# Kernel optimization log

Hardware: AMD Instinct MI355X
Metric: run time of the kernel (lower is better)

Reference implementation:

```python
import jax, jax.numpy as jnp
import numpy as np

N_NODES = 50000
N_EDGES = 800000
D = 96

def setup_inputs() -> dict:
    key = jax.random.key(0)
    ks = jax.random.split(key, 8)
    g = 0.1  # glorot-ish scale
    return {
        "x": jax.random.normal(ks[0], (N_NODES, D), jnp.float32),
        "edge_index": jax.random.randint(ks[1], (2, N_EDGES), 0, N_NODES, jnp.int64),
        "W1_root": jax.random.normal(ks[2], (D, D), jnp.float32) * g,
        "W1_nbr": jax.random.normal(ks[3], (D, D), jnp.float32) * g,
        "b1": jnp.zeros((D,), jnp.float32),
        "W2_root": jax.random.normal(ks[4], (D, D), jnp.float32) * g,
        "W2_nbr": jax.random.normal(ks[5], (D, D), jnp.float32) * g,
        "b2": jnp.zeros((D,), jnp.float32),
        "lin_w": jax.random.normal(ks[6], (D, 2 * D), jnp.float32) * g,
        "lin_b": jnp.zeros((D,), jnp.float32),
    }

def _conv(h, src, dst, W_root, W_nbr, b, neighbor_norm):
    # gather messages from source nodes, scatter-add into destination nodes
    agg = jax.ops.segment_sum(h[src], dst, num_segments=N_NODES)  # [N, D]
    if neighbor_norm:
        deg = jax.ops.segment_sum(jnp.ones_like(dst, dtype=h.dtype), dst,
                                  num_segments=N_NODES)
        agg = agg / jnp.maximum(deg, 1.0)[:, None]
    return h @ W_root + agg @ W_nbr + b

def reference(x, edge_index, W1_root, W1_nbr, b1, W2_root, W2_nbr, b2, lin_w, lin_b):
    src, dst = edge_index[0], edge_index[1]
    h1 = _conv(x, src, dst, W1_root, W1_nbr, b1, neighbor_norm=False)  # conv1, norm='None'
    h2 = _conv(h1, src, dst, W2_root, W2_nbr, b2, neighbor_norm=True)  # conv, neighbornorm
    # dropout is identity in eval mode; out=False so no global pooling
    cat = jnp.concatenate([h1, h2], axis=-1)  # [N, 2D]
    return jax.nn.relu(cat @ lin_w.T + lin_b)
```

## Files before the change

kernel.cpp:

```cpp
#include <hip/hip_runtime.h>

#define DN 96
#define NCHUNK 256

typedef __attribute__((ext_vector_type(8))) short bf16x8;
typedef __attribute__((ext_vector_type(4))) float f32x4;

__device__ __forceinline__ int edge_at(const void* ei, long long idx, int use64) {
    if (use64) return (int)((const long long*)ei)[idx];
    return ((const int*)ei)[idx];
}

__device__ __forceinline__ unsigned short f2bf(float f) {
    unsigned int u = __float_as_uint(f);
    return (unsigned short)((u + 0x7fffu + ((u >> 16) & 1u)) >> 16);
}

__global__ __launch_bounds__(256) void preprocess(
        const float* __restrict__ x, unsigned int* __restrict__ xb,
        const void* __restrict__ ei, unsigned int* __restrict__ eidx,
        int* __restrict__ hist,
        const float* __restrict__ W1r, const float* __restrict__ W1n,
        const float* __restrict__ W2r, const float* __restrict__ W2n,
        const float* __restrict__ lw, unsigned short* __restrict__ WT,
        long long E, long long CE, int nbuck, int NP) {
    __shared__ int lh[800];
    __shared__ int flag;
    int c = blockIdx.x, tid = threadIdx.x;

    if (tid == 0) flag = 1;
    for (int b = tid; b < nbuck; b += 256) lh[b] = 0;
    __syncthreads();
    if (((const unsigned int*)ei)[2 * tid + 1] != 0u) atomicAnd(&flag, 0);
    __syncthreads();
    int use64 = flag;

    long long beg = (long long)c * CE;
    long long end = beg + CE; if (end > E) end = E;
    for (long long e = beg + tid; e < end; e += 256) {
        int s = edge_at(ei, e, use64);
        int d = edge_at(ei, E + e, use64);
        eidx[e] = (unsigned int)s | ((unsigned int)d << 16);
        atomicAdd(&lh[d >> 6], 1);
    }
    __syncthreads();
    for (int b = tid; b < nbuck; b += 256)
        hist[(size_t)c * nbuck + b] = lh[b];

    int gstride = gridDim.x * 256;
    for (int i = c * 256 + tid; i < NP; i += gstride) {
        float2 v = *(const float2*)(x + 2 * (size_t)i);
        xb[i] = (unsigned int)f2bf(v.x) | ((unsigned int)f2bf(v.y) << 16);
    }

    for (int j = c * 256 + tid; j < 3 * DN * 192; j += gstride) {
        int w = j / (DN * 192);
        int r = j % (DN * 192);
        int jj = r / 192, k = r % 192;
        float v;
        if (w == 0)      v = (k < DN) ? W1r[(size_t)k * DN + jj] : W1n[(size_t)(k - DN) * DN + jj];
        else if (w == 1) v = (k < DN) ? W2r[(size_t)k * DN + jj] : W2n[(size_t)(k - DN) * DN + jj];
        else             v = lw[r];
        WT[j] = f2bf(v);
    }
}

__global__ void bucket_scan(const int* __restrict__ hist, int* __restrict__ pos_rel,
                            int* __restrict__ btot, int nbuck) {
    __shared__ int wsum[4];
    int b = blockIdx.x, tid = threadIdx.x;
    int lane = tid & 63, wid = tid >> 6;
    int v = hist[(size_t)tid * nbuck + b];
    int sv = v;
#pragma unroll
    for (int off = 1; off < 64; off <<= 1) {
        int t = __shfl_up(sv, off, 64);
        if (lane >= off) sv += t;
    }
    if (lane == 63) wsum[wid] = sv;
    __syncthreads();
    int woff = 0;
    for (int w = 0; w < wid; ++w) woff += wsum[w];
    pos_rel[(size_t)tid * nbuck + b] = woff + sv - v;
    if (tid == 255) btot[b] = woff + sv;
}

__global__ void scan_excl(int* data, int n) {
    __shared__ int swsum[16];
    int tid = threadIdx.x;
    int lane = tid & 63, wid = tid >> 6;
    int carry = 0;
    for (int base = 0; base < n; base += 1024) {
        int i = base + tid;
        int v = (i < n) ? data[i] : 0;
        int sv = v;
#pragma unroll
        for (int off = 1; off < 64; off <<= 1) {
            int t = __shfl_up(sv, off, 64);
            if (lane >= off) sv += t;
        }
        __syncthreads();
        if (lane == 63) swsum[wid] = sv;
        __syncthreads();
        if (tid < 16) {
            int wv = swsum[tid];
#pragma unroll
            for (int off = 1; off < 16; off <<= 1) {
                int t = __shfl_up(wv, off, 16);
                if (tid >= off) wv += t;
            }
            swsum[tid] = wv;
        }
        __syncthreads();
        int woff = (wid > 0) ? swsum[wid - 1] : 0;
        int excl = carry + woff + sv - v;
        if (i < n) data[i] = excl;
        carry += swsum[15];
        __syncthreads();
    }
    if (tid == 0) data[n] = carry;
}

__global__ void scatter_grouped(const unsigned int* __restrict__ eidx, long long E,
                                const int* __restrict__ pos_rel,
                                const int* __restrict__ bstart,
                                unsigned int* __restrict__ packed,
                                int nbuck, long long CE) {
    __shared__ int cur[800];
    int c = blockIdx.x, tid = threadIdx.x;
    for (int b = tid; b < nbuck; b += 256)
        cur[b] = pos_rel[(size_t)c * nbuck + b] + bstart[b];
    __syncthreads();
    long long beg = (long long)c * CE;
    long long end = beg + CE; if (end > E) end = E;
    for (long long e = beg + tid; e < end; e += 256) {
        unsigned int u = eidx[e];
        int src = (int)(u & 0xFFFFu);
        int dst = (int)(u >> 16);
        int b = dst >> 6;
        int p = atomicAdd(&cur[b], 1);
        packed[p] = (unsigned int)src | ((unsigned int)(dst & 63) << 16);
    }
}

__global__ void bucket_sort(const unsigned int* __restrict__ packed,
                            const int* __restrict__ bstart,
                            unsigned short* __restrict__ csr_src,
                            int* __restrict__ rowptr, int n, int nbuck) {
    __shared__ int bin[64];
    __shared__ int cur[64];
    int b = blockIdx.x, tid = threadIdx.x;
    int beg = bstart[b], end = bstart[b + 1];
    if (tid < 64) bin[tid] = 0;
    __syncthreads();
    for (int i = beg + tid; i < end; i += 256)
        atomicAdd(&bin[packed[i] >> 16], 1);
    __syncthreads();
    if (tid < 64) {
        int v = bin[tid];
        int sv = v;
#pragma unroll
        for (int off = 1; off < 64; off <<= 1) {
            int t = __shfl_up(sv, off, 64);
            if (tid >= off) sv += t;
        }
        int excl = sv - v;
        cur[tid] = beg + excl;
        int node = b * 64 + tid;
        if (node < n) rowptr[node] = beg + excl;
    }
    __syncthreads();
    for (int i = beg + tid; i < end; i += 256) {
        unsigned int p = packed[i];
        int q = atomicAdd(&cur[p >> 16], 1);
        csr_src[q] = (unsigned short)(p & 0xFFFFu);
    }
    if (b == nbuck - 1 && tid == 0) rowptr[n] = end;
}

__device__ __forceinline__ void acc_row(float* acc, uint4 v) {
    unsigned int u;
    u = v.x; acc[0] += __uint_as_float(u << 16); acc[1] += __uint_as_float(u & 0xffff0000u);
    u = v.y; acc[2] += __uint_as_float(u << 16); acc[3] += __uint_as_float(u & 0xffff0000u);
    u = v.z; acc[4] += __uint_as_float(u << 16); acc[5] += __uint_as_float(u & 0xffff0000u);
    u = v.w; acc[6] += __uint_as_float(u << 16); acc[7] += __uint_as_float(u & 0xffff0000u);
}

__global__ void aggregate(const unsigned int* __restrict__ in, unsigned int* __restrict__ out,
                          const int* __restrict__ rowptr,
                          const unsigned short* __restrict__ srcs,
                          int n, int normalize) {
    int t = blockIdx.x * blockDim.x + threadIdx.x;
    if (t >= n * 12) return;
    int node = t / 12, c = t % 12;
    int beg = rowptr[node], end = rowptr[node + 1];
    float acc[8];
#pragma unroll
    for (int j = 0; j < 8; ++j) acc[j] = 0.f;
    int i = beg;
    for (; i + 4 <= end; i += 4) {
        int s0 = srcs[i], s1 = srcs[i + 1], s2 = srcs[i + 2], s3 = srcs[i + 3];
        uint4 v0 = *(const uint4*)(in + (size_t)s0 * 48 + c * 4);
        uint4 v1 = *(const uint4*)(in + (size_t)s1 * 48 + c * 4);
        uint4 v2 = *(const uint4*)(in + (size_t)s2 * 48 + c * 4);
        uint4 v3 = *(const uint4*)(in + (size_t)s3 * 48 + c * 4);
        acc_row(acc, v0); acc_row(acc, v1); acc_row(acc, v2); acc_row(acc, v3);
    }
    for (; i < end; ++i) {
        uint4 v = *(const uint4*)(in + (size_t)srcs[i] * 48 + c * 4);
        acc_row(acc, v);
    }
    if (normalize) {
        float inv = 1.0f / fmaxf((float)(end - beg), 1.0f);
#pragma unroll
        for (int j = 0; j < 8; ++j) acc[j] *= inv;
    }
    uint4 r;
    r.x = (unsigned int)f2bf(acc[0]) | ((unsigned int)f2bf(acc[1]) << 16);
    r.y = (unsigned int)f2bf(acc[2]) | ((unsigned int)f2bf(acc[3]) << 16);
    r.z = (unsigned int)f2bf(acc[4]) | ((unsigned int)f2bf(acc[5]) << 16);
    r.w = (unsigned int)f2bf(acc[6]) | ((unsigned int)f2bf(acc[7]) << 16);
    *(uint4*)(out + (size_t)node * 48 + c * 4) = r;
}

__global__ __launch_bounds__(256) void gemm_mfma(
        const unsigned short* __restrict__ Abf, const unsigned short* __restrict__ Bbf,
        const unsigned short* __restrict__ WT, const float* __restrict__ bias,
        float* __restrict__ outf, unsigned short* __restrict__ outb,
        int n, int dorelu) {
    __shared__ unsigned int WTl[DN * 100];
    int tid = threadIdx.x;
    const unsigned int* WTg = (const unsigned int*)WT;
    for (int i = tid; i < DN * 96; i += 256) {
        int j = i / 96, m = i - j * 96;
        WTl[j * 100 + m] = WTg[i];
    }
    __syncthreads();

    int wid = tid >> 6, lane = tid & 63;
    int lg = lane >> 4, lr = lane & 15;
    int rowbase = blockIdx.x * 128 + wid * 32;

    f32x4 acc[2][6];
#pragma unroll
    for (int rt = 0; rt < 2; ++rt)
#pragma unroll
        for (int ct = 0; ct < 6; ++ct) acc[rt][ct] = (f32x4){0.f, 0.f, 0.f, 0.f};

    const unsigned short* WTs = (const unsigned short*)WTl;
#pragma unroll
    for (int kt = 0; kt < 6; ++kt) {
        const unsigned short* src = (kt < 3) ? Abf : Bbf;
        int kk = (kt < 3 ? kt : kt - 3) * 32 + lg * 8;
        bf16x8 afrag[2];
#pragma unroll
        for (int rt = 0; rt < 2; ++rt) {
            int row = rowbase + rt * 16 + lr;
            if (row >= n) row = n - 1;
            afrag[rt] = *(const bf16x8*)(src + (size_t)row * DN + kk);
        }
        int koff = kt * 32 + lg * 8;
#pragma unroll
        for (int ct = 0; ct < 6; ++ct) {
            bf16x8 bfrag = *(const bf16x8*)(WTs + (ct * 16 + lr) * 200 + koff);
            acc[0][ct] = __builtin_amdgcn_mfma_f32_16x16x32_bf16(afrag[0], bfrag, acc[0][ct], 0, 0, 0);
            acc[1][ct] = __builtin_amdgcn_mfma_f32_16x16x32_bf16(afrag[1], bfrag, acc[1][ct], 0, 0, 0);
        }
    }

#pragma unroll
    for (int ct = 0; ct < 6; ++ct) {
        int col = ct * 16 + lr;
        float bv = bias[col];
#pragma unroll
        for (int rt = 0; rt < 2; ++rt)
#pragma unroll
            for (int r = 0; r < 4; ++r) {
                int row = rowbase + rt * 16 + lg * 4 + r;
                if (row < n) {
                    float v = acc[rt][ct][r] + bv;
                    if (dorelu) v = fmaxf(v, 0.f);
                    if (outf) outf[(size_t)row * DN + col] = v;
                    if (outb) outb[(size_t)row * DN + col] = f2bf(v);
                }
            }
    }
}

__global__ __launch_bounds__(256) void gemm_fused(
        const unsigned short* __restrict__ h1, const unsigned short* __restrict__ agg,
        const unsigned short* __restrict__ WT2, const float* __restrict__ b2,
        const unsigned short* __restrict__ WT3, const float* __restrict__ lb,
        float* __restrict__ out, int n) {
    __shared__ unsigned int WTl[DN * 100];
    __shared__ unsigned short h2t[4][32][98];
    int tid = threadIdx.x, wid = tid >> 6, lane = tid & 63;
    int lg = lane >> 4, lr = lane & 15;
    int rowbase = blockIdx.x * 128 + wid * 32;

    const unsigned int* WTg2 = (const unsigned int*)WT2;
    for (int i = tid; i < DN * 96; i += 256) {
        int j = i / 96, m = i - j * 96;
        WTl[j * 100 + m] = WTg2[i];
    }
    __syncthreads();

    f32x4 acc[2][6];
#pragma unroll
    for (int rt = 0; rt < 2; ++rt)
#pragma unroll
        for (int ct = 0; ct < 6; ++ct) acc[rt][ct] = (f32x4){0.f, 0.f, 0.f, 0.f};

    const unsigned short* WTs = (const unsigned short*)WTl;
    bf16x8 afragA[2][3];
#pragma unroll
    for (int kt = 0; kt < 6; ++kt) {
        bf16x8 afrag[2];
#pragma unroll
        for (int rt = 0; rt < 2; ++rt) {
            int row = rowbase + rt * 16 + lr;
            if (row >= n) row = n - 1;
            if (kt < 3) {
                afrag[rt] = *(const bf16x8*)(h1 + (size_t)row * DN + kt * 32 + lg * 8);
                afragA[rt][kt] = afrag[rt];
            } else {
                afrag[rt] = *(const bf16x8*)(agg + (size_t)row * DN + (kt - 3) * 32 + lg * 8);
            }
        }
        int koff = kt * 32 + lg * 8;
#pragma unroll
        for (int ct = 0; ct < 6; ++ct) {
            bf16x8 bfrag = *(const bf16x8*)(WTs + (ct * 16 + lr) * 200 + koff);
            acc[0][ct] = __builtin_amdgcn_mfma_f32_16x16x32_bf16(afrag[0], bfrag, acc[0][ct], 0, 0, 0);
            acc[1][ct] = __builtin_amdgcn_mfma_f32_16x16x32_bf16(afrag[1], bfrag, acc[1][ct], 0, 0, 0);
        }
    }

#pragma unroll
    for (int ct = 0; ct < 6; ++ct) {
        float bv = b2[ct * 16 + lr];
#pragma unroll
        for (int rt = 0; rt < 2; ++rt)
#pragma unroll
            for (int r = 0; r < 4; ++r)
                h2t[wid][rt * 16 + lg * 4 + r][ct * 16 + lr] = f2bf(acc[rt][ct][r] + bv);
    }
    __syncthreads();

    const unsigned int* WTg3 = (const unsigned int*)WT3;
    for (int i = tid; i < DN * 96; i += 256) {
        int j = i / 96, m = i - j * 96;
        WTl[j * 100 + m] = WTg3[i];
    }
    __syncthreads();

    f32x4 acc2[2][6];
#pragma unroll
    for (int rt = 0; rt < 2; ++rt)
#pragma unroll
        for (int ct = 0; ct < 6; ++ct) acc2[rt][ct] = (f32x4){0.f, 0.f, 0.f, 0.f};

#pragma unroll
    for (int kt = 0; kt < 6; ++kt) {
        bf16x8 afrag[2];
#pragma unroll
        for (int rt = 0; rt < 2; ++rt) {
            if (kt < 3) afrag[rt] = afragA[rt][kt];
            else        afrag[rt] = *(const bf16x8*)(&h2t[wid][rt * 16 + lr][(kt - 3) * 32 + lg * 8]);
        }
        int koff = kt * 32 + lg * 8;
#pragma unroll
        for (int ct = 0; ct < 6; ++ct) {
            bf16x8 bfrag = *(const bf16x8*)(WTs + (ct * 16 + lr) * 200 + koff);
            acc2[0][ct] = __builtin_amdgcn_mfma_f32_16x16x32_bf16(afrag[0], bfrag, acc2[0][ct], 0, 0, 0);
            acc2[1][ct] = __builtin_amdgcn_mfma_f32_16x16x32_bf16(afrag[1], bfrag, acc2[1][ct], 0, 0, 0);
        }
    }

#pragma unroll
    for (int ct = 0; ct < 6; ++ct) {
        int col = ct * 16 + lr;
        float bv = lb[col];
#pragma unroll
        for (int rt = 0; rt < 2; ++rt)
#pragma unroll
            for (int r = 0; r < 4; ++r) {
                int row = rowbase + rt * 16 + lg * 4 + r;
                if (row < n)
                    out[(size_t)row * DN + col] = fmaxf(acc2[rt][ct][r] + bv, 0.f);
            }
    }
}

extern "C" void kernel_launch(void* const* d_in, const int* in_sizes, int n_in,
                              void* d_out, int out_size, void* d_ws, size_t ws_size,
                              hipStream_t stream) {
    const float* x   = (const float*)d_in[0];
    const void*  ei  = d_in[1];
    const float* W1r = (const float*)d_in[2];
    const float* W1n = (const float*)d_in[3];
    const float* b1  = (const float*)d_in[4];
    const float* W2r = (const float*)d_in[5];
    const float* W2n = (const float*)d_in[6];
    const float* b2  = (const float*)d_in[7];
    const float* lw  = (const float*)d_in[8];
    const float* lb  = (const float*)d_in[9];
    float* out = (float*)d_out;

    const int N = in_sizes[0] / DN;
    const long long E = in_sizes[1] / 2;
    const int NBUCK = (N + 63) / 64;
    const long long CE = (E + NCHUNK - 1) / NCHUNK;
    const size_t NP = (size_t)N * 48;

    unsigned int* xb   = (unsigned int*)d_ws;
    unsigned int* h1b  = xb + NP;
    unsigned int* aggb = h1b + NP;
    unsigned short* WT = (unsigned short*)(aggb + NP);
    unsigned short* WT1 = WT;
    unsigned short* WT2 = WT + DN * 192;
    unsigned short* WT3 = WT2 + DN * 192;
    unsigned int* eidx = (unsigned int*)(WT3 + DN * 192);
    int* hist   = (int*)(eidx + E);
    int* pos    = hist + NCHUNK * NBUCK;
    int* btot   = pos + NCHUNK * NBUCK;
    int* rowptr = btot + NBUCK + 1;
    unsigned int* packed = (unsigned int*)(rowptr + N + 1);
    unsigned short* csr_src = (unsigned short*)(packed + E);

    preprocess<<<NCHUNK, 256, 0, stream>>>(x, xb, ei, eidx, hist,
                                           W1r, W1n, W2r, W2n, lw, WT,
                                           E, CE, NBUCK, (int)NP);
    bucket_scan<<<NBUCK, 256, 0, stream>>>(hist, pos, btot, NBUCK);
    scan_excl<<<1, 1024, 0, stream>>>(btot, NBUCK);
    scatter_grouped<<<NCHUNK, 256, 0, stream>>>(eidx, E, pos, btot, packed, NBUCK, CE);
    bucket_sort<<<NBUCK, 256, 0, stream>>>(packed, btot, csr_src, rowptr, N, NBUCK);

    int ab = (N * 12 + 255) / 256;
    int gb = (N + 127) / 128;

    aggregate<<<ab, 256, 0, stream>>>(xb, aggb, rowptr, csr_src, N, 0);
    gemm_mfma<<<gb, 256, 0, stream>>>((const unsigned short*)xb, (const unsigned short*)aggb,
                                      WT1, b1, (float*)0, (unsigned short*)h1b, N, 0);
    aggregate<<<ab, 256, 0, stream>>>(h1b, aggb, rowptr, csr_src, N, 1);
    gemm_fused<<<gb, 256, 0, stream>>>((const unsigned short*)h1b, (const unsigned short*)aggb,
                                       WT2, b2, WT3, lb, out, N);
}
```

Baseline: 123.9 us.

## Assign one wavefront per node in aggregate and split edges across lane groups

The aggregate kernel now gives each node a full 64-lane wavefront. Five groups of 12 lanes each gather a strided subset of the node's edges, and the partial sums are reduced through shared memory. This adds memory-level parallelism for nodes with many neighbours and replaces the serial per-thread edge loop. Four lanes per wave sit idle and the reduction adds shared-memory traffic. Separately, preprocess launches 512 blocks so the bf16 conversion has more threads, and only the first NCHUNK blocks do the edge histogram.

```diff
diff --git a/kernel.cpp b/kernel.cpp
--- a/kernel.cpp
+++ b/kernel.cpp
@@ -35,17 +35,19 @@
     __syncthreads();
     int use64 = flag;
 
-    long long beg = (long long)c * CE;
-    long long end = beg + CE; if (end > E) end = E;
-    for (long long e = beg + tid; e < end; e += 256) {
-        int s = edge_at(ei, e, use64);
-        int d = edge_at(ei, E + e, use64);
-        eidx[e] = (unsigned int)s | ((unsigned int)d << 16);
-        atomicAdd(&lh[d >> 6], 1);
-    }
-    __syncthreads();
-    for (int b = tid; b < nbuck; b += 256)
-        hist[(size_t)c * nbuck + b] = lh[b];
+    if (c < NCHUNK) {
+        long long beg = (long long)c * CE;
+        long long end = beg + CE; if (end > E) end = E;
+        for (long long e = beg + tid; e < end; e += 256) {
+            int s = edge_at(ei, e, use64);
+            int d = edge_at(ei, E + e, use64);
+            eidx[e] = (unsigned int)s | ((unsigned int)d << 16);
+            atomicAdd(&lh[d >> 6], 1);
+        }
+        __syncthreads();
+        for (int b = tid; b < nbuck; b += 256)
+            hist[(size_t)c * nbuck + b] = lh[b];
+    }
 
     int gstride = gridDim.x * 256;
     for (int i = c * 256 + tid; i < NP; i += gstride) {
@@ -186,41 +188,56 @@
     u = v.w; acc[6] += __uint_as_float(u << 16); acc[7] += __uint_as_float(u & 0xffff0000u);
 }
 
-__global__ void aggregate(const unsigned int* __restrict__ in, unsigned int* __restrict__ out,
-                          const int* __restrict__ rowptr,
-                          const unsigned short* __restrict__ srcs,
-                          int n, int normalize) {
-    int t = blockIdx.x * blockDim.x + threadIdx.x;
-    if (t >= n * 12) return;
-    int node = t / 12, c = t % 12;
+__global__ __launch_bounds__(256) void aggregate(
+        const unsigned int* __restrict__ in, unsigned int* __restrict__ out,
+        const int* __restrict__ rowptr, const unsigned short* __restrict__ srcs,
+        int n, int normalize) {
+    __shared__ float red[4][64][8];
+    int wid = threadIdx.x >> 6, lane = threadIdx.x & 63;
+    int node = blockIdx.x * 4 + wid;
+    if (node >= n) return;
+    int c = lane % 12, eg = lane / 12;
     int beg = rowptr[node], end = rowptr[node + 1];
+
     float acc[8];
 #pragma unroll
     for (int j = 0; j < 8; ++j) acc[j] = 0.f;
-    int i = beg;
-    for (; i + 4 <= end; i += 4) {
-        int s0 = srcs[i], s1 = srcs[i + 1], s2 = srcs[i + 2], s3 = srcs[i + 3];
-        uint4 v0 = *(const uint4*)(in + (size_t)s0 * 48 + c * 4);
-        uint4 v1 = *(const uint4*)(in + (size_t)s1 * 48 + c * 4);
-        uint4 v2 = *(const uint4*)(in + (size_t)s2 * 48 + c * 4);
-        uint4 v3 = *(const uint4*)(in + (size_t)s3 * 48 + c * 4);
-        acc_row(acc, v0); acc_row(acc, v1); acc_row(acc, v2); acc_row(acc, v3);
-    }
-    for (; i < end; ++i) {
-        uint4 v = *(const uint4*)(in + (size_t)srcs[i] * 48 + c * 4);
-        acc_row(acc, v);
-    }
-    if (normalize) {
-        float inv = 1.0f / fmaxf((float)(end - beg), 1.0f);
-#pragma unroll
-        for (int j = 0; j < 8; ++j) acc[j] *= inv;
-    }
-    uint4 r;
-    r.x = (unsigned int)f2bf(acc[0]) | ((unsigned int)f2bf(acc[1]) << 16);
-    r.y = (unsigned int)f2bf(acc[2]) | ((unsigned int)f2bf(acc[3]) << 16);
-    r.z = (unsigned int)f2bf(acc[4]) | ((unsigned int)f2bf(acc[5]) << 16);
-    r.w = (unsigned int)f2bf(acc[6]) | ((unsigned int)f2bf(acc[7]) << 16);
-    *(uint4*)(out + (size_t)node * 48 + c * 4) = r;
+
+    if (eg < 5) {
+        int i = beg + eg;
+        for (; i + 5 < end; i += 10) {
+            int s0 = srcs[i], s1 = srcs[i + 5];
+            uint4 v0 = *(const uint4*)(in + (size_t)s0 * 48 + c * 4);
+            uint4 v1 = *(const uint4*)(in + (size_t)s1 * 48 + c * 4);
+            acc_row(acc, v0);
+            acc_row(acc, v1);
+        }
+        if (i < end) {
+            uint4 v = *(const uint4*)(in + (size_t)srcs[i] * 48 + c * 4);
+            acc_row(acc, v);
+        }
+    }
+
+#pragma unroll
+    for (int j = 0; j < 8; ++j) red[wid][lane][j] = acc[j];
+    asm volatile("s_waitcnt lgkmcnt(0)" ::: "memory");
+    if (eg == 0) {
+#pragma unroll
+        for (int k = 1; k < 5; ++k)
+#pragma unroll
+            for (int j = 0; j < 8; ++j) acc[j] += red[wid][c + 12 * k][j];
+        if (normalize) {
+            float inv = 1.0f / fmaxf((float)(end - beg), 1.0f);
+#pragma unroll
+            for (int j = 0; j < 8; ++j) acc[j] *= inv;
+        }
+        uint4 r;
+        r.x = (unsigned int)f2bf(acc[0]) | ((unsigned int)f2bf(acc[1]) << 16);
+        r.y = (unsigned int)f2bf(acc[2]) | ((unsigned int)f2bf(acc[3]) << 16);
+        r.z = (unsigned int)f2bf(acc[4]) | ((unsigned int)f2bf(acc[5]) << 16);
+        r.w = (unsigned int)f2bf(acc[6]) | ((unsigned int)f2bf(acc[7]) << 16);
+        *(uint4*)(out + (size_t)node * 48 + c * 4) = r;
+    }
 }
 
 __global__ __launch_bounds__(256) void gemm_mfma(
@@ -428,15 +445,15 @@
     unsigned int* packed = (unsigned int*)(rowptr + N + 1);
     unsigned short* csr_src = (unsigned short*)(packed + E);
 
-    preprocess<<<NCHUNK, 256, 0, stream>>>(x, xb, ei, eidx, hist,
-                                           W1r, W1n, W2r, W2n, lw, WT,
-                                           E, CE, NBUCK, (int)NP);
+    preprocess<<<512, 256, 0, stream>>>(x, xb, ei, eidx, hist,
+                                        W1r, W1n, W2r, W2n, lw, WT,
+                                        E, CE, NBUCK, (int)NP);
     bucket_scan<<<NBUCK, 256, 0, stream>>>(hist, pos, btot, NBUCK);
     scan_excl<<<1, 1024, 0, stream>>>(btot, NBUCK);
     scatter_grouped<<<NCHUNK, 256, 0, stream>>>(eidx, E, pos, btot, packed, NBUCK, CE);
     bucket_sort<<<NBUCK, 256, 0, stream>>>(packed, btot, csr_src, rowptr, N, NBUCK);
 
-    int ab = (N * 12 + 255) / 256;
+    int ab = (N + 3) / 4;
     int gb = (N + 127) / 128;
 
     aggregate<<<ab, 256, 0, stream>>>(xb, aggb, rowptr, csr_src, N, 0);
```

Result: no change. 124.2 us (+0.2%).
